# Kernel optimization log

Measured on AMD Instinct MI355X. Metric: run time of the kernel, lower is better.

Reference implementation:

```python
import jax, jax.numpy as jnp
import numpy as np

N_NODES = 100000
N_EDGES = 640000
N_LABEL = 100000
IN_C, HID_C, OUT_C = 128, 128, 64


def setup_inputs() -> dict:
    key = jax.random.key(0)
    ks = jax.random.split(key, 9)
    x = jax.random.normal(ks[0], (N_NODES, IN_C), dtype=jnp.float32)
    edge_index = jax.random.randint(ks[1], (2, N_EDGES), 0, N_NODES, dtype=jnp.int64)
    edge_label_index = jax.random.randint(ks[2], (2, N_LABEL), 0, N_NODES, dtype=jnp.int64)
    s = 0.05  # small init scale
    # PyG SAGEConv: lin_l applied to mean-aggregated neighbors (with bias), lin_r to root (no bias)
    W1l = jax.random.normal(ks[3], (HID_C, IN_C), dtype=jnp.float32) * s
    b1 = jnp.zeros((HID_C,), dtype=jnp.float32)
    W1r = jax.random.normal(ks[4], (HID_C, IN_C), dtype=jnp.float32) * s
    W2l = jax.random.normal(ks[5], (OUT_C, HID_C), dtype=jnp.float32) * s
    b2 = jnp.zeros((OUT_C,), dtype=jnp.float32)
    W2r = jax.random.normal(ks[6], (OUT_C, HID_C), dtype=jnp.float32) * s
    return {"x": x, "edge_index": edge_index, "edge_label_index": edge_label_index,
            "W1l": W1l, "b1": b1, "W1r": W1r, "W2l": W2l, "b2": b2, "W2r": W2r}


def _sage_conv(x, src, dst, Wl, b, Wr):
    # mean aggregation of source features at destination nodes
    agg = jax.ops.segment_sum(x[src], dst, num_segments=N_NODES)  # [N, d]
    cnt = jax.ops.segment_sum(jnp.ones((src.shape[0],), x.dtype), dst, num_segments=N_NODES)
    mean = agg / jnp.maximum(cnt, 1.0)[:, None]
    return mean @ Wl.T + b + x @ Wr.T


def reference(x, edge_index, edge_label_index, W1l, b1, W1r, W2l, b2, W2r):
    src, dst = edge_index[0], edge_index[1]
    h = jax.nn.relu(_sage_conv(x, src, dst, W1l, b1, W1r))
    z = _sage_conv(h, src, dst, W2l, b2, W2r)
    # edge-wise dot-product decode
    scores = jnp.sum(z[edge_label_index[0]] * z[edge_label_index[1]], axis=-1)  # [E_label]
    return scores
```

## Files before the change

### kernel.cpp

```cpp
#include <hip/hip_runtime.h>

#define N_NODES 100000
#define N_EDGES 640000
#define N_LABEL 100000
#define CAP 32

typedef __bf16 bf16x8 __attribute__((ext_vector_type(8)));
typedef float f32x4 __attribute__((ext_vector_type(4)));

#define CW1L 0
#define CB1  16384
#define CW1R 16512
#define CW2L 32896
#define CB2  41088
#define CW2R 41152
#define NWTS 49344

#define NB_W 193
#define NB_X 6250

__device__ __forceinline__ float bf2f(unsigned short u) {
    union { unsigned int i; float f; } c; c.i = ((unsigned int)u) << 16; return c.f;
}
__device__ __forceinline__ float asf(unsigned int u) {
    union { unsigned int i; float f; } c; c.i = u; return c.f;
}
__device__ __forceinline__ unsigned short f2bf(float f) {
    union { float f; unsigned int i; } c; c.f = f;
    unsigned int lsb = (c.i >> 16) & 1u;
    c.i += 0x7fffu + lsb;
    return (unsigned short)(c.i >> 16);
}

__global__ void k_init(const unsigned int* __restrict__ xw,
                       const unsigned int* __restrict__ eiw,
                       int* __restrict__ flags, int* __restrict__ cnt) {
    int i = blockIdx.x * blockDim.x + threadIdx.x;
    if (i < N_NODES) cnt[i] = 0;
    if (blockIdx.x == 0 && threadIdx.x < 64) {
        int l = threadIdx.x;
        unsigned int w = xw[l];
        unsigned short lo = (unsigned short)(w & 0xffffu);
        int e = (lo >> 7) & 0xff;
        bool bf_like = (lo == 0) || (e >= 98 && e <= 138);
        unsigned long long m = __ballot(bf_like);
        unsigned int ew = eiw[2 * l + 1];
        unsigned long long mz = __ballot(ew == 0u);
        if (l == 0) {
            flags[0] = (__popcll(m) < 48) ? 1 : 0;
            flags[1] = (__popcll(mz) == 64) ? 1 : 0;
        }
    }
}

__global__ void k_convwx(const void* W1l, const void* b1, const void* W1r,
                         const void* W2l, const void* b2, const void* W2r,
                         unsigned short* __restrict__ wts,
                         const void* __restrict__ x, unsigned short* __restrict__ xb,
                         const int* __restrict__ flags) {
    int b = blockIdx.x;
    int f32m = flags[0];
    if (b < NB_W) {
        int i = b * 256 + threadIdx.x;
        if (i >= NWTS) return;
        const void* src; int local;
        if      (i < CB1)  { src = W1l; local = i; }
        else if (i < CW1R) { src = b1;  local = i - CB1; }
        else if (i < CW2L) { src = W1r; local = i - CW1R; }
        else if (i < CB2)  { src = W2l; local = i - CW2L; }
        else if (i < CW2R) { src = b2;  local = i - CB2; }
        else               { src = W2r; local = i - CW2R; }
        wts[i] = f32m ? f2bf(((const float*)src)[local]) : ((const unsigned short*)src)[local];
    } else {
        int base = (b - NB_W) * 512 + threadIdx.x;
#pragma unroll
        for (int g = 0; g < 2; ++g) {
            int i = base + g * 256;
            if (i >= N_NODES * 32) continue;
            if (f32m) {
                float4 p = ((const float4*)x)[i];
                ushort4 o;
                o.x = f2bf(p.x); o.y = f2bf(p.y); o.z = f2bf(p.z); o.w = f2bf(p.w);
                ((ushort4*)xb)[i] = o;
            } else {
                ((ushort4*)xb)[i] = ((const ushort4*)x)[i];
            }
        }
    }
}

__global__ void k_fill(const int* __restrict__ ei, int* __restrict__ cnt,
                       int* __restrict__ csr, const int* __restrict__ flags) {
    int e = blockIdx.x * blockDim.x + threadIdx.x;
    if (e >= N_EDGES) return;
    int i64 = flags[1];
    int src = ei[e << i64], dst = ei[(N_EDGES + e) << i64];
    int pos = atomicAdd(&cnt[dst], 1);
    if (pos < CAP) csr[dst * CAP + pos] = src;
}

__global__ __launch_bounds__(256) void k_fused1(
    const int* __restrict__ cnt, const int* __restrict__ csr,
    const unsigned short* __restrict__ xb, const unsigned short* __restrict__ wts,
    unsigned short* __restrict__ tbl, unsigned short* __restrict__ tbr)
{
    __shared__ unsigned short sm[32][136];
    int wave = threadIdx.x >> 6, lane = threadIdx.x & 63;
    int nb0 = blockIdx.x * 32;

    {
        int nA = nb0 + wave * 8;
        int half = lane >> 5, sl = lane & 31;
        int rows[4];
#pragma unroll
        for (int p = 0; p < 4; ++p)
            rows[p] = csr[(size_t)(nA + p * 2 + half) * CAP + sl];
        int dpre = (lane < 8) ? cnt[nA + lane] : 0;
        int c2 = lane << 1;

#pragma unroll
        for (int j = 0; j < 8; ++j) {
            int deg = __shfl(dpre, j);
            int m = deg < CAP ? deg : CAP;
            float s0 = 0.f, s1 = 0.f;
            for (int e0 = 0; e0 < m; e0 += 8) {
                unsigned int v[8];
#pragma unroll
                for (int u = 0; u < 8; ++u) {
                    int e = e0 + u;
                    int sidx = __shfl(rows[j >> 1], (j & 1) * 32 + e);
                    sidx = (e < m) ? sidx : 0;
                    v[u] = *(const unsigned int*)(xb + (size_t)sidx * 128 + c2);
                }
#pragma unroll
                for (int u = 0; u < 8; ++u) {
                    unsigned int w = ((e0 + u) < m) ? v[u] : 0u;
                    s0 += asf(w << 16);
                    s1 += asf(w & 0xffff0000u);
                }
            }
            float inv = 1.0f / (deg > 1 ? (float)deg : 1.0f);
            unsigned int o = (unsigned int)f2bf(s0 * inv) | ((unsigned int)f2bf(s1 * inv) << 16);
            *(unsigned int*)&sm[wave * 8 + j][c2] = o;
        }
    }
    __syncthreads();

    int qq = wave;
    int row = lane & 15, kq = lane >> 4;
    int col = lane & 15, rq = lane >> 4;
    f32x4 acc[2][2];
    {
        bf16x8 Wf[16];
#pragma unroll
        for (int t = 0; t < 2; ++t)
#pragma unroll
            for (int ks = 0; ks < 8; ++ks) {
                const int k0 = ks * 32;
                const unsigned short* base = wts + (k0 < 128 ? CW1L : CW1R)
                    + (size_t)(qq * 32 + t * 16 + row) * 128 + (k0 & 127) + kq * 8;
                Wf[t * 8 + ks] = *reinterpret_cast<const bf16x8*>(base);
            }
#pragma unroll
        for (int i = 0; i < 2; ++i) {
            bf16x8 Af[8];
#pragma unroll
            for (int ks = 0; ks < 4; ++ks)
                Af[ks] = *reinterpret_cast<const bf16x8*>(&sm[i * 16 + row][ks * 32 + kq * 8]);
            const unsigned short* rx = xb + (size_t)(nb0 + i * 16 + row) * 128 + kq * 8;
#pragma unroll
            for (int ks = 0; ks < 4; ++ks)
                Af[4 + ks] = *reinterpret_cast<const bf16x8*>(rx + ks * 32);
            acc[i][0] = (f32x4){0.f, 0.f, 0.f, 0.f};
            acc[i][1] = (f32x4){0.f, 0.f, 0.f, 0.f};
#pragma unroll
            for (int ks = 0; ks < 8; ++ks) {
                acc[i][0] = __builtin_amdgcn_mfma_f32_16x16x32_bf16(Af[ks], Wf[ks],     acc[i][0], 0, 0, 0);
                acc[i][1] = __builtin_amdgcn_mfma_f32_16x16x32_bf16(Af[ks], Wf[8 + ks], acc[i][1], 0, 0, 0);
            }
        }
    }
    __syncthreads();
    {
        float bias0 = bf2f(wts[CB1 + qq * 32 + col]);
        float bias1 = bf2f(wts[CB1 + qq * 32 + 16 + col]);
#pragma unroll
        for (int i = 0; i < 2; ++i)
#pragma unroll
            for (int r = 0; r < 4; ++r) {
                int nl = i * 16 + rq * 4 + r;
                float v0 = acc[i][0][r] + bias0; v0 = v0 > 0.f ? v0 : 0.f;
                float v1 = acc[i][1][r] + bias1; v1 = v1 > 0.f ? v1 : 0.f;
                sm[nl][qq * 32 + col]      = f2bf(v0);
                sm[nl][qq * 32 + 16 + col] = f2bf(v1);
            }
    }
    __syncthreads();

    {
        const size_t wbase = (qq < 2) ? (CW2L + (size_t)(qq * 32) * 128)
                                      : (CW2R + (size_t)((qq - 2) * 32) * 128);
        bf16x8 Wg[8];
#pragma unroll
        for (int t = 0; t < 2; ++t)
#pragma unroll
            for (int ks = 0; ks < 4; ++ks)
                Wg[t * 4 + ks] = *reinterpret_cast<const bf16x8*>(
                    wts + wbase + (size_t)(t * 16 + row) * 128 + ks * 32 + kq * 8);
        unsigned short* dst = (qq < 2) ? tbl : tbr;
        int cb = (qq & 1) * 32;
#pragma unroll
        for (int i = 0; i < 2; ++i) {
            bf16x8 Ag[4];
#pragma unroll
            for (int ks = 0; ks < 4; ++ks)
                Ag[ks] = *reinterpret_cast<const bf16x8*>(&sm[i * 16 + row][ks * 32 + kq * 8]);
            f32x4 c0 = (f32x4){0.f, 0.f, 0.f, 0.f};
            f32x4 c1 = (f32x4){0.f, 0.f, 0.f, 0.f};
#pragma unroll
            for (int ks = 0; ks < 4; ++ks) {
                c0 = __builtin_amdgcn_mfma_f32_16x16x32_bf16(Ag[ks], Wg[ks],     c0, 0, 0, 0);
                c1 = __builtin_amdgcn_mfma_f32_16x16x32_bf16(Ag[ks], Wg[4 + ks], c1, 0, 0, 0);
            }
#pragma unroll
            for (int r = 0; r < 4; ++r) {
                int n = nb0 + i * 16 + rq * 4 + r;
                dst[(size_t)n * 64 + cb + col]      = f2bf(c0[r]);
                dst[(size_t)n * 64 + cb + 16 + col] = f2bf(c1[r]);
            }
        }
    }
}

__global__ __launch_bounds__(256) void k_agg2c(
    const int* __restrict__ cnt, const int* __restrict__ csr,
    const unsigned short* __restrict__ tbl, const unsigned short* __restrict__ tbr,
    const unsigned short* __restrict__ wts, unsigned short* __restrict__ zb) {
    int wv = (int)((blockIdx.x * blockDim.x + threadIdx.x) >> 6);
    int n2 = wv * 2;
    if (n2 >= N_NODES) return;
    int lane = threadIdx.x & 63;
    int half = lane >> 5, sl = lane & 31;
    int n = n2 + half;
    int dpre = (lane < 2) ? cnt[n2 + lane] : 0;
    int deg = __shfl(dpre, half);
    int m = deg < CAP ? deg : CAP;
    int mo = __shfl(m, lane ^ 32);
    int mmax = m > mo ? m : mo;
    int srcrow = csr[(size_t)n * CAP + sl];
    int c2 = sl << 1;
    float s0 = 0.f, s1 = 0.f;
    for (int e0 = 0; e0 < mmax; e0 += 8) {
        unsigned int v[8];
#pragma unroll
        for (int u = 0; u < 8; ++u) {
            int e = e0 + u;
            int sidx = __shfl(srcrow, half * 32 + e);
            sidx = (e < m) ? sidx : 0;
            v[u] = *(const unsigned int*)(tbl + (size_t)sidx * 64 + c2);
        }
#pragma unroll
        for (int u = 0; u < 8; ++u) {
            unsigned int w = ((e0 + u) < m) ? v[u] : 0u;
            s0 += asf(w << 16);
            s1 += asf(w & 0xffff0000u);
        }
    }
    float inv = 1.0f / (deg > 1 ? (float)deg : 1.0f);
    unsigned int tr = *(const unsigned int*)(tbr + (size_t)n * 64 + c2);
    unsigned int bb = *(const unsigned int*)(wts + CB2 + c2);
    float zx = s0 * inv + asf(bb << 16)          + asf(tr << 16);
    float zy = s1 * inv + asf(bb & 0xffff0000u)  + asf(tr & 0xffff0000u);
    unsigned int o = (unsigned int)f2bf(zx) | ((unsigned int)f2bf(zy) << 16);
    *(unsigned int*)(zb + (size_t)n * 64 + c2) = o;
}

__global__ void k_decode(const int* __restrict__ eli, const unsigned short* __restrict__ zb,
                         void* __restrict__ out, const int* __restrict__ flags) {
    long long t = (long long)blockIdx.x * blockDim.x + threadIdx.x;
    int e = (int)(t >> 3);
    if (e >= N_LABEL) return;
    int f32m = flags[0], i64 = flags[1];
    int q = threadIdx.x & 7;
    int a = eli[e << i64], b = eli[(N_LABEL + e) << i64];
    uint4 pa = *(const uint4*)(zb + (size_t)a * 64 + q * 8);
    uint4 pb = *(const uint4*)(zb + (size_t)b * 64 + q * 8);
    float s = asf(pa.x << 16) * asf(pb.x << 16) + asf(pa.x & 0xffff0000u) * asf(pb.x & 0xffff0000u)
            + asf(pa.y << 16) * asf(pb.y << 16) + asf(pa.y & 0xffff0000u) * asf(pb.y & 0xffff0000u)
            + asf(pa.z << 16) * asf(pb.z << 16) + asf(pa.z & 0xffff0000u) * asf(pb.z & 0xffff0000u)
            + asf(pa.w << 16) * asf(pb.w << 16) + asf(pa.w & 0xffff0000u) * asf(pb.w & 0xffff0000u);
#pragma unroll
    for (int off = 1; off < 8; off <<= 1) s += __shfl_xor(s, off);
    if (q == 0) {
        if (f32m) ((float*)out)[e] = s;
        else      ((unsigned short*)out)[e] = f2bf(s);
    }
}

extern "C" void kernel_launch(void* const* d_in, const int* in_sizes, int n_in,
                              void* d_out, int out_size, void* d_ws, size_t ws_size,
                              hipStream_t stream) {
    const void* x   = d_in[0];
    const int*  ei  = (const int*)d_in[1];
    const int*  eli = (const int*)d_in[2];
    const void* W1l = d_in[3];
    const void* b1  = d_in[4];
    const void* W1r = d_in[5];
    const void* W2l = d_in[6];
    const void* b2  = d_in[7];
    const void* W2r = d_in[8];

    char* ws = (char*)d_ws;
    const size_t offFlag = 0;
    const size_t offCnt  = 1024;
    const size_t offWts  = 801024;
    const size_t offCsr  = 1u << 20;
    const size_t offXb   = offCsr + (size_t)N_NODES * CAP * 4;
    const size_t offTbl  = offXb  + (size_t)N_NODES * 128 * 2;
    const size_t offTbr  = offTbl + (size_t)N_NODES * 64 * 2;
    const size_t offZb   = offTbr + (size_t)N_NODES * 64 * 2;

    int*            flags = (int*)(ws + offFlag);
    int*            cnt   = (int*)(ws + offCnt);
    unsigned short* wts   = (unsigned short*)(ws + offWts);
    int*            csr   = (int*)(ws + offCsr);
    unsigned short* xb    = (unsigned short*)(ws + offXb);
    unsigned short* tbl   = (unsigned short*)(ws + offTbl);
    unsigned short* tbr   = (unsigned short*)(ws + offTbr);
    unsigned short* zb    = (unsigned short*)(ws + offZb);

    k_init<<<(N_NODES + 255) / 256, 256, 0, stream>>>((const unsigned int*)x,
                                                      (const unsigned int*)ei, flags, cnt);

    k_convwx<<<NB_W + NB_X, 256, 0, stream>>>(W1l, b1, W1r, W2l, b2, W2r, wts, x, xb, flags);

    k_fill<<<(N_EDGES + 255) / 256, 256, 0, stream>>>(ei, cnt, csr, flags);

    k_fused1<<<N_NODES / 32, 256, 0, stream>>>(cnt, csr, xb, wts, tbl, tbr);

    k_agg2c<<<12500, 256, 0, stream>>>(cnt, csr, tbl, tbr, wts, zb);

    k_decode<<<(N_LABEL * 8) / 256, 256, 0, stream>>>(eli, zb, d_out, flags);
}
```

Measured before the change: 232.6 us.

## Merge init into prep kernel and process four nodes per wave in layer-2 aggregation

The separate init kernel is folded into the weight/feature conversion kernel, and every kernel now recomputes the dtype detection flags itself by wave ballot instead of reading a flags buffer. This removes one launch and the dependency on the flags buffer. The layer-2 aggregation now handles four nodes per wave with 16 lanes each, loading 4 bf16 values per lane, so the block count is halved and each neighbour gather issues wider loads. In exchange, every wave repeats the detection reads, and the loop bound is now per-group, which can cause divergence inside a wave.

```diff
diff --git a/kernel.cpp b/kernel.cpp
--- a/kernel.cpp
+++ b/kernel.cpp
@@ -16,6 +16,7 @@
 #define CW2R 41152
 #define NWTS 49344
 
+#define NB_C 391
 #define NB_W 193
 #define NB_X 6250
 
@@ -32,36 +33,32 @@
     return (unsigned short)(c.i >> 16);
 }
 
-__global__ void k_init(const unsigned int* __restrict__ xw,
-                       const unsigned int* __restrict__ eiw,
-                       int* __restrict__ flags, int* __restrict__ cnt) {
-    int i = blockIdx.x * blockDim.x + threadIdx.x;
-    if (i < N_NODES) cnt[i] = 0;
-    if (blockIdx.x == 0 && threadIdx.x < 64) {
-        int l = threadIdx.x;
-        unsigned int w = xw[l];
-        unsigned short lo = (unsigned short)(w & 0xffffu);
-        int e = (lo >> 7) & 0xff;
-        bool bf_like = (lo == 0) || (e >= 98 && e <= 138);
-        unsigned long long m = __ballot(bf_like);
-        unsigned int ew = eiw[2 * l + 1];
-        unsigned long long mz = __ballot(ew == 0u);
-        if (l == 0) {
-            flags[0] = (__popcll(m) < 48) ? 1 : 0;
-            flags[1] = (__popcll(mz) == 64) ? 1 : 0;
-        }
-    }
-}
-
-__global__ void k_convwx(const void* W1l, const void* b1, const void* W1r,
-                         const void* W2l, const void* b2, const void* W2r,
-                         unsigned short* __restrict__ wts,
-                         const void* __restrict__ x, unsigned short* __restrict__ xb,
-                         const int* __restrict__ flags) {
+__device__ __forceinline__ void detect(const void* x, const int* ei, int& f32m, int& i64) {
+    int lane = threadIdx.x & 63;
+    unsigned int w = ((const unsigned int*)x)[lane];
+    unsigned short lo = (unsigned short)(w & 0xffffu);
+    int e = (lo >> 7) & 0xff;
+    bool bf_like = (lo == 0) || (e >= 98 && e <= 138);
+    f32m = (__popcll(__ballot(bf_like)) < 48) ? 1 : 0;
+    unsigned int ew = ((const unsigned int*)ei)[2 * lane + 1];
+    i64 = (__popcll(__ballot(ew == 0u)) == 64) ? 1 : 0;
+}
+
+__global__ void k_prep(const void* W1l, const void* b1, const void* W1r,
+                       const void* W2l, const void* b2, const void* W2r,
+                       unsigned short* __restrict__ wts,
+                       const void* __restrict__ x, unsigned short* __restrict__ xb,
+                       const int* __restrict__ ei, int* __restrict__ cnt) {
     int b = blockIdx.x;
-    int f32m = flags[0];
-    if (b < NB_W) {
+    if (b < NB_C) {
         int i = b * 256 + threadIdx.x;
+        if (i < N_NODES) cnt[i] = 0;
+        return;
+    }
+    int f32m, i64;
+    detect(x, ei, f32m, i64);
+    if (b < NB_C + NB_W) {
+        int i = (b - NB_C) * 256 + threadIdx.x;
         if (i >= NWTS) return;
         const void* src; int local;
         if      (i < CB1)  { src = W1l; local = i; }
@@ -72,7 +69,7 @@
         else               { src = W2r; local = i - CW2R; }
         wts[i] = f32m ? f2bf(((const float*)src)[local]) : ((const unsigned short*)src)[local];
     } else {
-        int base = (b - NB_W) * 512 + threadIdx.x;
+        int base = (b - NB_C - NB_W) * 512 + threadIdx.x;
 #pragma unroll
         for (int g = 0; g < 2; ++g) {
             int i = base + g * 256;
@@ -90,10 +87,11 @@
 }
 
 __global__ void k_fill(const int* __restrict__ ei, int* __restrict__ cnt,
-                       int* __restrict__ csr, const int* __restrict__ flags) {
+                       int* __restrict__ csr, const void* __restrict__ x) {
+    int f32m, i64;
+    detect(x, ei, f32m, i64);
     int e = blockIdx.x * blockDim.x + threadIdx.x;
     if (e >= N_EDGES) return;
-    int i64 = flags[1];
     int src = ei[e << i64], dst = ei[(N_EDGES + e) << i64];
     int pos = atomicAdd(&cnt[dst], 1);
     if (pos < CAP) csr[dst * CAP + pos] = src;
@@ -117,7 +115,6 @@
             rows[p] = csr[(size_t)(nA + p * 2 + half) * CAP + sl];
         int dpre = (lane < 8) ? cnt[nA + lane] : 0;
         int c2 = lane << 1;
-
 #pragma unroll
         for (int j = 0; j < 8; ++j) {
             int deg = __shfl(dpre, j);
@@ -237,50 +234,61 @@
     const unsigned short* __restrict__ tbl, const unsigned short* __restrict__ tbr,
     const unsigned short* __restrict__ wts, unsigned short* __restrict__ zb) {
     int wv = (int)((blockIdx.x * blockDim.x + threadIdx.x) >> 6);
-    int n2 = wv * 2;
-    if (n2 >= N_NODES) return;
+    int n4 = wv * 4;
+    if (n4 >= N_NODES) return;
     int lane = threadIdx.x & 63;
-    int half = lane >> 5, sl = lane & 31;
-    int n = n2 + half;
-    int dpre = (lane < 2) ? cnt[n2 + lane] : 0;
-    int deg = __shfl(dpre, half);
+    int g16 = lane >> 4, sl = lane & 15;
+    int n = n4 + g16;
+    int dpre = (lane < 4) ? cnt[n4 + lane] : 0;
+    int deg = __shfl(dpre, g16);
     int m = deg < CAP ? deg : CAP;
-    int mo = __shfl(m, lane ^ 32);
-    int mmax = m > mo ? m : mo;
-    int srcrow = csr[(size_t)n * CAP + sl];
-    int c2 = sl << 1;
-    float s0 = 0.f, s1 = 0.f;
-    for (int e0 = 0; e0 < mmax; e0 += 8) {
-        unsigned int v[8];
+    int srcA = csr[(size_t)n * CAP + sl];
+    int srcB = csr[(size_t)n * CAP + 16 + sl];
+    int c4 = sl << 2;
+    float s0 = 0.f, s1 = 0.f, s2 = 0.f, s3 = 0.f;
+    for (int e0 = 0; e0 < m; e0 += 8) {
+        uint2 v[8];
 #pragma unroll
         for (int u = 0; u < 8; ++u) {
             int e = e0 + u;
-            int sidx = __shfl(srcrow, half * 32 + e);
+            int ia = __shfl(srcA, g16 * 16 + (e & 15));
+            int ib = __shfl(srcB, g16 * 16 + (e & 15));
+            int sidx = (e < 16) ? ia : ib;
             sidx = (e < m) ? sidx : 0;
-            v[u] = *(const unsigned int*)(tbl + (size_t)sidx * 64 + c2);
+            v[u] = *(const uint2*)(tbl + (size_t)sidx * 64 + c4);
         }
 #pragma unroll
         for (int u = 0; u < 8; ++u) {
-            unsigned int w = ((e0 + u) < m) ? v[u] : 0u;
-            s0 += asf(w << 16);
-            s1 += asf(w & 0xffff0000u);
+            bool ok = (e0 + u) < m;
+            unsigned int wx = ok ? v[u].x : 0u;
+            unsigned int wy = ok ? v[u].y : 0u;
+            s0 += asf(wx << 16);
+            s1 += asf(wx & 0xffff0000u);
+            s2 += asf(wy << 16);
+            s3 += asf(wy & 0xffff0000u);
         }
     }
     float inv = 1.0f / (deg > 1 ? (float)deg : 1.0f);
-    unsigned int tr = *(const unsigned int*)(tbr + (size_t)n * 64 + c2);
-    unsigned int bb = *(const unsigned int*)(wts + CB2 + c2);
-    float zx = s0 * inv + asf(bb << 16)          + asf(tr << 16);
-    float zy = s1 * inv + asf(bb & 0xffff0000u)  + asf(tr & 0xffff0000u);
-    unsigned int o = (unsigned int)f2bf(zx) | ((unsigned int)f2bf(zy) << 16);
-    *(unsigned int*)(zb + (size_t)n * 64 + c2) = o;
+    uint2 tr = *(const uint2*)(tbr + (size_t)n * 64 + c4);
+    uint2 bb = *(const uint2*)(wts + CB2 + c4);
+    float z0 = s0 * inv + asf(bb.x << 16)         + asf(tr.x << 16);
+    float z1 = s1 * inv + asf(bb.x & 0xffff0000u) + asf(tr.x & 0xffff0000u);
+    float z2 = s2 * inv + asf(bb.y << 16)         + asf(tr.y << 16);
+    float z3 = s3 * inv + asf(bb.y & 0xffff0000u) + asf(tr.y & 0xffff0000u);
+    uint2 o;
+    o.x = (unsigned int)f2bf(z0) | ((unsigned int)f2bf(z1) << 16);
+    o.y = (unsigned int)f2bf(z2) | ((unsigned int)f2bf(z3) << 16);
+    *(uint2*)(zb + (size_t)n * 64 + c4) = o;
 }
 
 __global__ void k_decode(const int* __restrict__ eli, const unsigned short* __restrict__ zb,
-                         void* __restrict__ out, const int* __restrict__ flags) {
+                         void* __restrict__ out, const void* __restrict__ x,
+                         const int* __restrict__ ei) {
+    int f32m, i64;
+    detect(x, ei, f32m, i64);
     long long t = (long long)blockIdx.x * blockDim.x + threadIdx.x;
     int e = (int)(t >> 3);
     if (e >= N_LABEL) return;
-    int f32m = flags[0], i64 = flags[1];
     int q = threadIdx.x & 7;
     int a = eli[e << i64], b = eli[(N_LABEL + e) << i64];
     uint4 pa = *(const uint4*)(zb + (size_t)a * 64 + q * 8);
@@ -311,7 +319,6 @@
     const void* W2r = d_in[8];
 
     char* ws = (char*)d_ws;
-    const size_t offFlag = 0;
     const size_t offCnt  = 1024;
     const size_t offWts  = 801024;
     const size_t offCsr  = 1u << 20;
@@ -320,7 +327,6 @@
     const size_t offTbr  = offTbl + (size_t)N_NODES * 64 * 2;
     const size_t offZb   = offTbr + (size_t)N_NODES * 64 * 2;
 
-    int*            flags = (int*)(ws + offFlag);
     int*            cnt   = (int*)(ws + offCnt);
     unsigned short* wts   = (unsigned short*)(ws + offWts);
     int*            csr   = (int*)(ws + offCsr);
@@ -329,16 +335,14 @@
     unsigned short* tbr   = (unsigned short*)(ws + offTbr);
     unsigned short* zb    = (unsigned short*)(ws + offZb);
 
-    k_init<<<(N_NODES + 255) / 256, 256, 0, stream>>>((const unsigned int*)x,
-                                                      (const unsigned int*)ei, flags, cnt);
-
-    k_convwx<<<NB_W + NB_X, 256, 0, stream>>>(W1l, b1, W1r, W2l, b2, W2r, wts, x, xb, flags);
-
-    k_fill<<<(N_EDGES + 255) / 256, 256, 0, stream>>>(ei, cnt, csr, flags);
+    k_prep<<<NB_C + NB_W + NB_X, 256, 0, stream>>>(W1l, b1, W1r, W2l, b2, W2r,
+                                                   wts, x, xb, ei, cnt);
+
+    k_fill<<<(N_EDGES + 255) / 256, 256, 0, stream>>>(ei, cnt, csr, x);
 
     k_fused1<<<N_NODES / 32, 256, 0, stream>>>(cnt, csr, xb, wts, tbl, tbr);
 
-    k_agg2c<<<12500, 256, 0, stream>>>(cnt, csr, tbl, tbr, wts, zb);
-
-    k_decode<<<(N_LABEL * 8) / 256, 256, 0, stream>>>(eli, zb, d_out, flags);
-}
+    k_agg2c<<<6250, 256, 0, stream>>>(cnt, csr, tbl, tbr, wts, zb);
+
+    k_decode<<<(N_LABEL * 8) / 256, 256, 0, stream>>>(eli, zb, d_out, x, ei);
+}
```

New measurement: 227.0 us. -2.4%, faster.
